# Kernel tuning notes

Hardware: AMD Instinct MI355X
Metric: run time of the kernel (lower is better)

Reference implementation:

```python
import jax, jax.numpy as jnp
import numpy as np

N_ATOMS = 100000
ATOM_FDIM = 133
HIDDEN = 512
MAX_NEI = 6
N_MOLS = 4096
N_PAIRS = 8192


def setup_inputs() -> dict:
    key = jax.random.key(0)
    ks = jax.random.split(key, 12)
    s = 0.05  # weight init scale
    return {
        'f_atoms': jax.random.normal(ks[0], (N_ATOMS, ATOM_FDIM), jnp.float32),
        'a_neighbors': jax.random.randint(ks[1], (N_ATOMS, MAX_NEI), 0, N_ATOMS, dtype=jnp.int32),
        'mol_ids': jnp.sort(jax.random.randint(ks[2], (N_ATOMS,), 0, N_MOLS, dtype=jnp.int32)),
        'batch_edges': jax.random.randint(ks[3], (2, N_PAIRS), 0, N_MOLS, dtype=jnp.int32),
        'W_i': jax.random.normal(ks[4], (ATOM_FDIM, HIDDEN), jnp.float32) * s,
        'W_h': jax.random.normal(ks[5], (HIDDEN, HIDDEN), jnp.float32) * s,
        'W_o': jax.random.normal(ks[6], (ATOM_FDIM + HIDDEN, HIDDEN), jnp.float32) * s,
        'b_o': jnp.zeros((HIDDEN,), jnp.float32),
        'W_ffn_i': jax.random.normal(ks[7], (4 * HIDDEN, 2048), jnp.float32) * s,
        'b_ffn_i': jnp.zeros((2048,), jnp.float32),
        'W_ffn_1': jax.random.normal(ks[8], (2048, 1024), jnp.float32) * s,
        'b_ffn_1': jnp.zeros((1024,), jnp.float32),
        'W_ffn_2': jax.random.normal(ks[9], (1024, 1), jnp.float32) * s,
        'b_ffn_2': jnp.zeros((1,), jnp.float32),
    }


def reference(f_atoms, a_neighbors, mol_ids, batch_edges,
              W_i, W_h, W_o, b_o,
              W_ffn_i, b_ffn_i, W_ffn_1, b_ffn_1, W_ffn_2, b_ffn_2):
    # input = W_i(f_atoms); message = relu(input)
    inp = f_atoms @ W_i                      # [N, H]
    message = jax.nn.relu(inp)
    # neighbor gather + sum aggregation
    message = jnp.take(message, a_neighbors, axis=0).sum(axis=1)  # [N, H]
    # single message-passing layer (n_message_layer = 1), dropout=0 -> identity
    message = jax.nn.relu(inp + message @ W_h)
    # second gather + sum, then readout projection
    a_message = jnp.take(message, a_neighbors, axis=0).sum(axis=1)  # [N, H]
    a_input = jnp.concatenate([f_atoms, a_message], axis=1)         # [N, F+H]
    atom_hiddens = jax.nn.relu(a_input @ W_o + b_o)                 # [N, H]
    # segment-mean readout per molecule (empty segments -> zero vector)
    sums = jax.ops.segment_sum(atom_hiddens, mol_ids, num_segments=N_MOLS)
    counts = jax.ops.segment_sum(jnp.ones((atom_hiddens.shape[0], 1), atom_hiddens.dtype),
                                 mol_ids, num_segments=N_MOLS)
    mol_vecs = sums / jnp.maximum(counts, 1.0)                      # [M, H]
    # pairwise drug-drug features
    e1 = mol_vecs[batch_edges[0]]
    e2 = mol_vecs[batch_edges[1]]
    feature = jnp.concatenate([e1 + e2, e1 * e2, e1, e2], axis=1)   # [P, 4H]
    h = feature @ W_ffn_i + b_ffn_i
    h = jax.nn.relu(h) @ W_ffn_1 + b_ffn_1
    h = jax.nn.relu(h) @ W_ffn_2 + b_ffn_2
    return jax.nn.sigmoid(h).reshape(-1)                            # [P]
```

## Files before the change

### kernel.cpp

```cpp
#include <hip/hip_runtime.h>
#include <math.h>

#define N_ATOMS   100000
#define ATOM_FDIM 133
#define HIDDEN    512
#define MAX_NEI   6
#define N_MOLS    4096
#define N_PAIRS   8192

typedef __attribute__((ext_vector_type(8))) short short8;
typedef __attribute__((ext_vector_type(4))) float f32x4;
typedef __attribute__((ext_vector_type(2))) float f32x2;
typedef __attribute__((ext_vector_type(8))) int int8v;

static __device__ __forceinline__ float bf2f(unsigned short h) {
    return __uint_as_float(((unsigned int)h) << 16);
}
static __device__ __forceinline__ unsigned short f2bf(float f) {
    unsigned int u = __float_as_uint(f);
    u += 0x7FFFu + ((u >> 16) & 1u);
    return (unsigned short)(u >> 16);
}
static __device__ __forceinline__ unsigned int pk2bf(float a, float b) {
    unsigned int ua = __float_as_uint(a); ua += 0x7FFFu + ((ua >> 16) & 1u);
    unsigned int ub = __float_as_uint(b); ub += 0x7FFFu + ((ub >> 16) & 1u);
    return (ua >> 16) | (ub & 0xFFFF0000u);
}
static __device__ __forceinline__ unsigned int pk4f8(float a, float b, float c, float d) {
    unsigned int r = 0;
    r = __builtin_amdgcn_cvt_pk_fp8_f32(a, b, r, false);
    r = __builtin_amdgcn_cvt_pk_fp8_f32(c, d, r, true);
    return r;
}
static __device__ __forceinline__ void gl_lds16(const void* g, void* l) {
    __builtin_amdgcn_global_load_lds(
        (__attribute__((address_space(1))) void*)g,
        (__attribute__((address_space(3))) void*)l, 16, 0, 0);
}

__global__ __launch_bounds__(256)
void convert_f8(const float* __restrict__ in, unsigned char* __restrict__ out)
{
    int v = blockIdx.x * 256 + threadIdx.x;
    int row = v >> 4, sl = v & 15;
    int k0 = sl * 16;
    bool rok = row < N_ATOMS;
    const float* r = in + (size_t)row * ATOM_FDIM;
    float f[16];
#pragma unroll
    for (int e = 0; e < 16; ++e) {
        int kk = k0 + e;
        f[e] = (rok && kk < ATOM_FDIM) ? r[kk] : 0.f;
    }
    uint4 u;
    u.x = pk4f8(f[0], f[1], f[2], f[3]);
    u.y = pk4f8(f[4], f[5], f[6], f[7]);
    u.z = pk4f8(f[8], f[9], f[10], f[11]);
    u.w = pk4f8(f[12], f[13], f[14], f[15]);
    *(uint4*)(out + (size_t)row * 256 + k0) = u;
}

template<bool HAS_A0, bool RELU, bool HAS_BIAS, bool HAS_ADD, bool SWZ>
__global__ __launch_bounds__(256)
void gemm_f8(const unsigned char* __restrict__ A0, int lda0, int K0p,
             const unsigned char* __restrict__ A2, int lda2, int Kp,
             const unsigned char* __restrict__ Bt,
             const float* __restrict__ bias,
             const unsigned char* __restrict__ addm,
             unsigned char* __restrict__ C, int M, int N)
{
    __shared__ unsigned char lds[128 * 256];
    unsigned char* As = lds;
    unsigned char* Bs = lds + 128 * 128;
    unsigned short* Ct = (unsigned short*)lds;

    const int tid  = threadIdx.x;
    const int lane = tid & 63;
    const int wid  = tid >> 6;
    int bx, by;
    if (SWZ) {
        int L = blockIdx.y * gridDim.x + blockIdx.x;
        int xcd = L & 7, s = L >> 3;
        bx = s % gridDim.x;
        by = xcd + 8 * (s / gridDim.x);
    } else { bx = blockIdx.x; by = blockIdx.y; }
    const int row0 = by * 128;
    const int col0 = bx * 128;
    const int wm   = wid & 1, wn = wid >> 1;
    const int quad = lane >> 4, l15 = lane & 15;
    const int srow = lane >> 3, schunk = lane & 7;
    const int ssw  = (schunk ^ srow) * 16;

    f32x4 acc[4][4];
#pragma unroll
    for (int i = 0; i < 4; ++i)
#pragma unroll
        for (int j = 0; j < 4; ++j)
#pragma unroll
            for (int r = 0; r < 4; ++r) acc[i][j][r] = 0.f;

    for (int k0 = 0; k0 < Kp; k0 += 128) {
        __syncthreads();
        const unsigned char* Ak;
        int akof, alda;
        if (HAS_A0 && k0 < K0p) { Ak = A0; akof = k0; alda = lda0; }
        else { Ak = A2; akof = HAS_A0 ? (k0 - K0p) : k0; alda = lda2; }
#pragma unroll
        for (int i = 0; i < 4; ++i) {
            int mbase = wid * 32 + i * 8;
            int r = row0 + mbase + srow;
            gl_lds16(Ak + (size_t)r * alda + akof + ssw, &As[mbase * 128]);
        }
#pragma unroll
        for (int i = 0; i < 4; ++i) {
            int nbase = wid * 32 + i * 8;
            int rn = col0 + nbase + srow;
            gl_lds16(Bt + (size_t)rn * Kp + k0 + ssw, &Bs[nbase * 128]);
        }
        __syncthreads();
        const int s0 = ((2 * quad) ^ (l15 & 7)) * 16;
        const int s1 = ((2 * quad + 1) ^ (l15 & 7)) * 16;
        int8v a[4], b[4];
#pragma unroll
        for (int mt = 0; mt < 4; ++mt) {
            int r = wm * 64 + mt * 16 + l15;
            uint4 lo = *(const uint4*)&As[r * 128 + s0];
            uint4 hi = *(const uint4*)&As[r * 128 + s1];
            a[mt][0] = lo.x; a[mt][1] = lo.y; a[mt][2] = lo.z; a[mt][3] = lo.w;
            a[mt][4] = hi.x; a[mt][5] = hi.y; a[mt][6] = hi.z; a[mt][7] = hi.w;
        }
#pragma unroll
        for (int nt = 0; nt < 4; ++nt) {
            int r = wn * 64 + nt * 16 + l15;
            uint4 lo = *(const uint4*)&Bs[r * 128 + s0];
            uint4 hi = *(const uint4*)&Bs[r * 128 + s1];
            b[nt][0] = lo.x; b[nt][1] = lo.y; b[nt][2] = lo.z; b[nt][3] = lo.w;
            b[nt][4] = hi.x; b[nt][5] = hi.y; b[nt][6] = hi.z; b[nt][7] = hi.w;
        }
#pragma unroll
        for (int mt = 0; mt < 4; ++mt)
#pragma unroll
            for (int nt = 0; nt < 4; ++nt)
                acc[mt][nt] = __builtin_amdgcn_mfma_scale_f32_16x16x128_f8f6f4(
                    a[mt], b[nt], acc[mt][nt], 0, 0, 0, 127, 0, 127);
    }

    __syncthreads();
#pragma unroll
    for (int mt = 0; mt < 4; ++mt)
#pragma unroll
        for (int nt = 0; nt < 4; ++nt) {
            int cbase = wn * 64 + nt * 16 + l15;
            int rbase = wm * 64 + mt * 16 + quad * 4;
#pragma unroll
            for (int r = 0; r < 4; ++r)
                Ct[(rbase + r) * 128 + cbase] = f2bf(acc[mt][nt][r]);
        }
    __syncthreads();
#pragma unroll
    for (int i = 0; i < 8; ++i) {
        int c = tid + i * 256;
        int rr = c >> 4, cc = (c & 15) * 8;
        int m = row0 + rr, n = col0 + cc;
        short8 v = *(const short8*)&Ct[rr * 128 + cc];
        float f[8];
#pragma unroll
        for (int q = 0; q < 8; ++q) f[q] = bf2f((unsigned short)v[q]);
        if (HAS_BIAS) {
            float4 b0 = *(const float4*)(bias + n);
            float4 b1 = *(const float4*)(bias + n + 4);
            f[0] += b0.x; f[1] += b0.y; f[2] += b0.z; f[3] += b0.w;
            f[4] += b1.x; f[5] += b1.y; f[6] += b1.z; f[7] += b1.w;
        }
        if (m < M) {
            if (HAS_ADD) {
                uint2 ad = *(const uint2*)(addm + (size_t)m * N + n);
                f32x2 p;
                p = __builtin_amdgcn_cvt_pk_f32_fp8(ad.x, false); f[0] += p.x; f[1] += p.y;
                p = __builtin_amdgcn_cvt_pk_f32_fp8(ad.x, true);  f[2] += p.x; f[3] += p.y;
                p = __builtin_amdgcn_cvt_pk_f32_fp8(ad.y, false); f[4] += p.x; f[5] += p.y;
                p = __builtin_amdgcn_cvt_pk_f32_fp8(ad.y, true);  f[6] += p.x; f[7] += p.y;
            }
            if (RELU)
#pragma unroll
                for (int q = 0; q < 8; ++q) f[q] = fmaxf(f[q], 0.f);
            uint2 o;
            o.x = pk4f8(f[0], f[1], f[2], f[3]);
            o.y = pk4f8(f[4], f[5], f[6], f[7]);
            *(uint2*)(C + (size_t)m * N + n) = o;
        }
    }
}

template<int NT, bool RELU, bool HAS_BIAS>
__global__ __launch_bounds__(512, 2)
void gemm_bt2(const unsigned short* __restrict__ A, int lda, int Kp,
              const unsigned short* __restrict__ Bt,
              const float* __restrict__ bias,
              unsigned short* __restrict__ C, int M, int N)
{
    constexpr int BN = NT * 64;
    constexpr int SMEM = 2 * 256 * 64 * 2 + 2 * BN * 64 * 2;
    __shared__ unsigned char smem[SMEM];
    unsigned short* As_ = (unsigned short*)smem;
    unsigned short* Bs_ = (unsigned short*)(smem + 2 * 256 * 64 * 2);
    unsigned short* Ct  = (unsigned short*)smem;

    const int tid  = threadIdx.x;
    const int lane = tid & 63;
    const int wid  = tid >> 6;
    const int wr   = wid >> 2;
    const int wc   = wid & 3;
    const int quad = lane >> 4, l15 = lane & 15;
    const int srow = lane >> 3, schunk = lane & 7;
    const int ssw  = (schunk ^ srow) * 8;

    const int row0 = blockIdx.y * 256;
    const int col0 = blockIdx.x * BN;

    f32x4 acc[8][NT];
#pragma unroll
    for (int i = 0; i < 8; ++i)
#pragma unroll
        for (int j = 0; j < NT; ++j)
#pragma unroll
            for (int r = 0; r < 4; ++r) acc[i][j][r] = 0.f;

#define STAGE_TILE(t, d)                                                     \
    {                                                                        \
        const int k0s = (t) * 64;                                            \
        _Pragma("unroll")                                                    \
        for (int i = 0; i < 4; ++i) {                                        \
            int mbase = wid * 32 + i * 8;                                    \
            int r = row0 + mbase + srow;                                     \
            gl_lds16(A + (size_t)r * lda + k0s + ssw,                        \
                     As_ + (d) * (256 * 64) + mbase * 64);                   \
        }                                                                    \
        _Pragma("unroll")                                                    \
        for (int i = 0; i < NT; ++i) {                                       \
            int nbase = wid * (NT * 8) + i * 8;                              \
            int rn = col0 + nbase + srow;                                    \
            gl_lds16(Bt + (size_t)rn * Kp + k0s + ssw,                       \
                     Bs_ + (d) * (BN * 64) + nbase * 64);                    \
        }                                                                    \
    }

    const int slot0 = ((quad) ^ (l15 & 7)) * 8;
    const int slot1 = ((4 + quad) ^ (l15 & 7)) * 8;

    const int ntiles = Kp >> 6;
    STAGE_TILE(0, 0);
    __syncthreads();

    for (int t = 0; t < ntiles; ++t) {
        const int d = t & 1;
        if (t + 1 < ntiles) STAGE_TILE(t + 1, d ^ 1);

        const int abase = d * (256 * 64);
        const int bbase = d * (BN * 64);
        short8 bf[NT][2];
#pragma unroll
        for (int nt2 = 0; nt2 < NT; ++nt2) {
            int cn = wc * (NT * 16) + nt2 * 16 + l15;
            bf[nt2][0] = *(const short8*)&Bs_[bbase + cn * 64 + slot0];
            bf[nt2][1] = *(const short8*)&Bs_[bbase + cn * 64 + slot1];
        }
#pragma unroll
        for (int q = 0; q < 4; ++q) {
            short8 af[2][2];
#pragma unroll
            for (int j = 0; j < 2; ++j) {
                int ar = wr * 128 + (q * 2 + j) * 16 + l15;
                af[j][0] = *(const short8*)&As_[abase + ar * 64 + slot0];
                af[j][1] = *(const short8*)&As_[abase + ar * 64 + slot1];
            }
            __builtin_amdgcn_s_setprio(1);
#pragma unroll
            for (int j = 0; j < 2; ++j)
#pragma unroll
                for (int nt2 = 0; nt2 < NT; ++nt2) {
                    acc[q * 2 + j][nt2] = __builtin_amdgcn_mfma_f32_16x16x32_bf16(
                        af[j][0], bf[nt2][0], acc[q * 2 + j][nt2], 0, 0, 0);
                    acc[q * 2 + j][nt2] = __builtin_amdgcn_mfma_f32_16x16x32_bf16(
                        af[j][1], bf[nt2][1], acc[q * 2 + j][nt2], 0, 0, 0);
                }
            __builtin_amdgcn_s_setprio(0);
        }
        __syncthreads();
    }
#undef STAGE_TILE

#pragma unroll
    for (int mt = 0; mt < 8; ++mt)
#pragma unroll
        for (int nt2 = 0; nt2 < NT; ++nt2) {
            int cbase = wc * (NT * 16) + nt2 * 16 + l15;
            int rbase = wr * 128 + mt * 16 + quad * 4;
#pragma unroll
            for (int r = 0; r < 4; ++r)
                Ct[(rbase + r) * BN + cbase] = f2bf(acc[mt][nt2][r]);
        }
    __syncthreads();
    constexpr int NSTORE = 256 * BN / (512 * 8);
#pragma unroll
    for (int i = 0; i < NSTORE; ++i) {
        int idx = (i * 512 + tid) * 8;
        int rr = idx / BN, cc = idx % BN;
        int m = row0 + rr, n = col0 + cc;
        short8 v = *(const short8*)&Ct[rr * BN + cc];
        float f[8];
#pragma unroll
        for (int q = 0; q < 8; ++q) f[q] = bf2f((unsigned short)v[q]);
        if (HAS_BIAS) {
            float4 b0 = *(const float4*)(bias + n);
            float4 b1 = *(const float4*)(bias + n + 4);
            f[0] += b0.x; f[1] += b0.y; f[2] += b0.z; f[3] += b0.w;
            f[4] += b1.x; f[5] += b1.y; f[6] += b1.z; f[7] += b1.w;
        }
        if (RELU)
#pragma unroll
            for (int q = 0; q < 8; ++q) f[q] = fmaxf(f[q], 0.f);
        uint4 o;
        o.x = pk2bf(f[0], f[1]); o.y = pk2bf(f[2], f[3]);
        o.z = pk2bf(f[4], f[5]); o.w = pk2bf(f[6], f[7]);
        *(uint4*)(C + (size_t)m * N + n) = o;
    }
    (void)M;
}

__global__ __launch_bounds__(256)
void transpose_bf16(const float* __restrict__ in, int K, int N,
                    unsigned short* __restrict__ out, int ldOut, int Kz, int koff)
{
    __shared__ float t[32][33];
    const int n0 = blockIdx.x * 32, k0 = blockIdx.y * 32;
    const int tx = threadIdx.x & 31, ty = threadIdx.x >> 5;
#pragma unroll
    for (int i = 0; i < 32; i += 8) {
        int k = k0 + ty + i, n = n0 + tx;
        t[ty + i][tx] = (k < K && n < N) ? in[(size_t)k * N + n] : 0.f;
    }
    __syncthreads();
#pragma unroll
    for (int i = 0; i < 32; i += 8) {
        int n = n0 + ty + i, k = k0 + tx;
        if (n < N && k < Kz)
            out[(size_t)n * ldOut + koff + k] = f2bf(t[tx][ty + i]);
    }
}

__global__ __launch_bounds__(256)
void transpose_f8(const float* __restrict__ in, int K, int N,
                  unsigned char* __restrict__ out, int ldOut, int Kz, int koff)
{
    __shared__ float t[32][33];
    const int n0 = blockIdx.x * 32, k0 = blockIdx.y * 32;
    const int tx = threadIdx.x & 31, ty = threadIdx.x >> 5;
#pragma unroll
    for (int i = 0; i < 32; i += 8) {
        int k = k0 + ty + i, n = n0 + tx;
        t[ty + i][tx] = (k < K && n < N) ? in[(size_t)k * N + n] : 0.f;
    }
    __syncthreads();
#pragma unroll
    for (int i = 0; i < 32; i += 8) {
        int n = n0 + ty + i, k = k0 + tx;
        if (n < N && k < Kz) {
            float v = t[tx][ty + i];
            out[(size_t)n * ldOut + koff + k] =
                (unsigned char)(__builtin_amdgcn_cvt_pk_fp8_f32(v, v, 0, false) & 0xFF);
        }
    }
}

__global__ __launch_bounds__(256)
void transpose_add_bf16(const float* __restrict__ inA, const float* __restrict__ inB,
                        int K, int N, unsigned short* __restrict__ out,
                        int ldOut, int koff)
{
    __shared__ float t[32][33];
    const int n0 = blockIdx.x * 32, k0 = blockIdx.y * 32;
    const int tx = threadIdx.x & 31, ty = threadIdx.x >> 5;
#pragma unroll
    for (int i = 0; i < 32; i += 8) {
        int k = k0 + ty + i, n = n0 + tx;
        float v = 0.f;
        if (k < K && n < N) {
            v = inA[(size_t)k * N + n];
            if (inB) v += inB[(size_t)k * N + n];
        }
        t[ty + i][tx] = v;
    }
    __syncthreads();
#pragma unroll
    for (int i = 0; i < 32; i += 8) {
        int n = n0 + ty + i, k = k0 + tx;
        if (n < N && k < K)
            out[(size_t)n * ldOut + koff + k] = f2bf(t[tx][ty + i]);
    }
}

template<bool RELU>
__global__ __launch_bounds__(256)
void gather_f8(const unsigned char* __restrict__ src,
               const int* __restrict__ nei, unsigned char* __restrict__ dst)
{
    const int atom = blockIdx.x * 8 + (threadIdx.x >> 5);
    const int l32  = threadIdx.x & 31;
    const int off  = l32 * 16;
    const int* np_ = nei + (size_t)atom * MAX_NEI;
    float s[16];
#pragma unroll
    for (int e = 0; e < 16; ++e) s[e] = 0.f;
#pragma unroll
    for (int j = 0; j < MAX_NEI; ++j) {
        uint4 u = *(const uint4*)(src + (size_t)np_[j] * HIDDEN + off);
        unsigned int w[4] = {u.x, u.y, u.z, u.w};
#pragma unroll
        for (int q = 0; q < 4; ++q) {
            f32x2 lo = __builtin_amdgcn_cvt_pk_f32_fp8(w[q], false);
            f32x2 hi = __builtin_amdgcn_cvt_pk_f32_fp8(w[q], true);
            float v0 = lo.x, v1 = lo.y, v2 = hi.x, v3 = hi.y;
            if (RELU) {
                v0 = fmaxf(v0, 0.f); v1 = fmaxf(v1, 0.f);
                v2 = fmaxf(v2, 0.f); v3 = fmaxf(v3, 0.f);
            }
            s[4 * q] += v0; s[4 * q + 1] += v1; s[4 * q + 2] += v2; s[4 * q + 3] += v3;
        }
    }
    uint4 o;
    o.x = pk4f8(s[0], s[1], s[2], s[3]);
    o.y = pk4f8(s[4], s[5], s[6], s[7]);
    o.z = pk4f8(s[8], s[9], s[10], s[11]);
    o.w = pk4f8(s[12], s[13], s[14], s[15]);
    *(uint4*)(dst + (size_t)atom * HIDDEN + off) = o;
}

__global__ __launch_bounds__(256)
void segmean_f8(const unsigned char* __restrict__ H,
                const int* __restrict__ mol_ids, float* __restrict__ molv)
{
    const int m = blockIdx.x;
    const int d = threadIdx.x * 2;
    int lo = 0, hi = N_ATOMS;
    while (lo < hi) { int mid = (lo + hi) >> 1; if (mol_ids[mid] < m) lo = mid + 1; else hi = mid; }
    const int start = lo;
    hi = N_ATOMS;
    while (lo < hi) { int mid = (lo + hi) >> 1; if (mol_ids[mid] < m + 1) lo = mid + 1; else hi = mid; }
    const int end = lo;
    float s0 = 0.f, s1 = 0.f;
    for (int a = start; a < end; ++a) {
        unsigned int raw = *(const unsigned short*)(H + (size_t)a * HIDDEN + d);
        f32x2 f = __builtin_amdgcn_cvt_pk_f32_fp8(raw, false);
        s0 += f.x; s1 += f.y;
    }
    int cnt = end - start;
    float inv = 1.0f / (float)(cnt > 0 ? cnt : 1);
    float2 o; o.x = s0 * inv; o.y = s1 * inv;
    *(float2*)(molv + (size_t)m * HIDDEN + d) = o;
}

__global__ __launch_bounds__(128)
void feature_kernel(const float* __restrict__ molv, const int* __restrict__ edges,
                    unsigned short* __restrict__ feat)
{
    const int p  = blockIdx.x;
    const int d4 = threadIdx.x * 4;
    const int i  = edges[p];
    const int j  = edges[N_PAIRS + p];
    float4 a = *(const float4*)(molv + (size_t)i * HIDDEN + d4);
    float4 b = *(const float4*)(molv + (size_t)j * HIDDEN + d4);
    unsigned short* o = feat + (size_t)p * 1536;
    uint2 w;
    w.x = pk2bf(a.x, a.y); w.y = pk2bf(a.z, a.w);
    *(uint2*)(o + d4) = w;
    w.x = pk2bf(b.x, b.y); w.y = pk2bf(b.z, b.w);
    *(uint2*)(o + HIDDEN + d4) = w;
    w.x = pk2bf(a.x * b.x, a.y * b.y); w.y = pk2bf(a.z * b.z, a.w * b.w);
    *(uint2*)(o + 2 * HIDDEN + d4) = w;
}

__global__ __launch_bounds__(256)
void final_kernel(const unsigned short* __restrict__ H, const float* __restrict__ w,
                  const float* __restrict__ b, float* __restrict__ out)
{
    const int p   = blockIdx.x;
    const int tid = threadIdx.x;
    const unsigned short* row = H + (size_t)p * 1024;
    float s = 0.f;
    for (int i = tid; i < 1024; i += 256) s += bf2f(row[i]) * w[i];
#pragma unroll
    for (int off = 32; off > 0; off >>= 1) s += __shfl_down(s, off, 64);
    __shared__ float red[4];
    if ((tid & 63) == 0) red[tid >> 6] = s;
    __syncthreads();
    if (tid == 0) {
        float t = red[0] + red[1] + red[2] + red[3] + b[0];
        out[p] = 1.0f / (1.0f + expf(-t));
    }
}

extern "C" void kernel_launch(void* const* d_in, const int* in_sizes, int n_in,
                              void* d_out, int out_size, void* d_ws, size_t ws_size,
                              hipStream_t stream)
{
    const float* f_atoms = (const float*)d_in[0];
    const int*   a_nei   = (const int*)d_in[1];
    const int*   mol_ids = (const int*)d_in[2];
    const int*   edges   = (const int*)d_in[3];
    const float* W_i     = (const float*)d_in[4];
    const float* W_h     = (const float*)d_in[5];
    const float* W_o     = (const float*)d_in[6];
    const float* b_o     = (const float*)d_in[7];
    const float* W_ffn_i = (const float*)d_in[8];
    const float* b_ffn_i = (const float*)d_in[9];
    const float* W_ffn_1 = (const float*)d_in[10];
    const float* b_ffn_1 = (const float*)d_in[11];
    const float* W_ffn_2 = (const float*)d_in[12];
    const float* b_ffn_2 = (const float*)d_in[13];
    float* out = (float*)d_out;

    char* ws = (char*)d_ws;
    unsigned char*  I     = (unsigned char*)ws;
    unsigned char*  Y     = (unsigned char*)(ws + 51200000);
    unsigned char*  Wt_i  = (unsigned char*)(ws + 102400000);
    unsigned char*  Wch   = (unsigned char*)(ws + 102531072);
    unsigned char*  Wco   = (unsigned char*)(ws + 102793216);
    float*          Mv    = (float*)(ws + 103186432);
    unsigned short* Wt_f0 = (unsigned short*)(ws + 111575040);
    unsigned short* Wt_f1 = (unsigned short*)(ws + 117866496);
    unsigned short* F     = (unsigned short*)(ws + 122060800);
    unsigned short* H1    = (unsigned short*)(ws + 147226624);
    unsigned short* H2    = (unsigned short*)(ws + 180781056);
    unsigned char*  Xf8   = (unsigned char*)(ws + 122060800);

    const float* W0 = W_ffn_i;
    const float* W1 = W_ffn_i + (size_t)512 * 2048;
    const float* W2 = W_ffn_i + (size_t)1024 * 2048;
    const float* W3 = W_ffn_i + (size_t)1536 * 2048;

    transpose_f8<<<dim3(16, 8),  256, 0, stream>>>(W_i, 133, 512, Wt_i, 256, 256, 0);
    transpose_f8<<<dim3(16, 16), 256, 0, stream>>>(W_h, 512, 512, Wch, 512, 512, 0);
    transpose_f8<<<dim3(16, 8),  256, 0, stream>>>(W_o, 133, 512, Wco, 768, 256, 0);
    transpose_f8<<<dim3(16, 16), 256, 0, stream>>>(W_o + (size_t)133 * 512,
                                                   512, 512, Wco, 768, 512, 256);
    transpose_add_bf16<<<dim3(64, 16), 256, 0, stream>>>(W0, W2, 512, 2048, Wt_f0, 1536, 0);
    transpose_add_bf16<<<dim3(64, 16), 256, 0, stream>>>(W0, W3, 512, 2048, Wt_f0, 1536, 512);
    transpose_add_bf16<<<dim3(64, 16), 256, 0, stream>>>(W1, nullptr, 512, 2048, Wt_f0, 1536, 1024);
    transpose_bf16<<<dim3(32, 64), 256, 0, stream>>>(W_ffn_1, 2048, 1024, Wt_f1, 2048, 2048, 0);

    convert_f8<<<100352 * 16 / 256, 256, 0, stream>>>(f_atoms, Xf8);

    gemm_f8<true, false, false, false, true><<<dim3(4, 784), 256, 0, stream>>>(
        Xf8, 256, 256, nullptr, 0, 256, Wt_i, nullptr, nullptr, I, N_ATOMS, HIDDEN);
    gather_f8<true><<<N_ATOMS / 8, 256, 0, stream>>>(I, a_nei, Y);
    gemm_f8<false, true, false, true, true><<<dim3(4, 784), 256, 0, stream>>>(
        nullptr, 0, 0, Y, 512, 512, Wch, nullptr, I, I, N_ATOMS, HIDDEN);
    gather_f8<false><<<N_ATOMS / 8, 256, 0, stream>>>(I, a_nei, Y);
    gemm_f8<true, true, true, false, true><<<dim3(4, 784), 256, 0, stream>>>(
        Xf8, 256, 256, Y, 512, 768, Wco, b_o, nullptr, I, N_ATOMS, HIDDEN);
    segmean_f8<<<N_MOLS, 256, 0, stream>>>(I, mol_ids, Mv);
    feature_kernel<<<N_PAIRS, 128, 0, stream>>>(Mv, edges, F);
    gemm_bt2<4, true, true><<<dim3(8, 32), 512, 0, stream>>>(
        F, 1536, 1536, Wt_f0, b_ffn_i, H1, N_PAIRS, 2048);
    gemm_bt2<2, true, true><<<dim3(8, 32), 512, 0, stream>>>(
        H1, 2048, 2048, Wt_f1, b_ffn_1, H2, N_PAIRS, 1024);
    final_kernel<<<N_PAIRS, 256, 0, stream>>>(H2, W_ffn_2, b_ffn_2, out);
    (void)in_sizes; (void)n_in; (void)out_size; (void)ws_size;
}
```

Before: 540.3 us.

## Double-buffer FP8 GEMM LDS tiles and remap bf16 GEMM blocks across XCDs

The FP8 GEMM now double-buffers its A/B LDS tiles (64KB), prefetching the next K tile while MFMAs run on the current one, with one barrier per iteration instead of two. It raises wave priority around the MFMA block and pads the bf16 output staging tile stride to 136 to reduce LDS bank conflicts. The bf16 GEMM remaps linear block IDs so consecutive tiles land on the same XCD for L2 locality. Doubling LDS use may lower occupancy, and the XCD remap assumes the grid size is divisible by 8.

```diff
diff --git a/kernel.cpp b/kernel.cpp
--- a/kernel.cpp
+++ b/kernel.cpp
@@ -69,9 +69,9 @@
              const unsigned char* __restrict__ addm,
              unsigned char* __restrict__ C, int M, int N)
 {
-    __shared__ unsigned char lds[128 * 256];
+    __shared__ unsigned char lds[65536];
     unsigned char* As = lds;
-    unsigned char* Bs = lds + 128 * 128;
+    unsigned char* Bs = lds + 32768;
     unsigned short* Ct = (unsigned short*)lds;
 
     const int tid  = threadIdx.x;
@@ -99,53 +99,70 @@
 #pragma unroll
             for (int r = 0; r < 4; ++r) acc[i][j][r] = 0.f;
 
-    for (int k0 = 0; k0 < Kp; k0 += 128) {
-        __syncthreads();
-        const unsigned char* Ak;
-        int akof, alda;
-        if (HAS_A0 && k0 < K0p) { Ak = A0; akof = k0; alda = lda0; }
-        else { Ak = A2; akof = HAS_A0 ? (k0 - K0p) : k0; alda = lda2; }
-#pragma unroll
-        for (int i = 0; i < 4; ++i) {
-            int mbase = wid * 32 + i * 8;
-            int r = row0 + mbase + srow;
-            gl_lds16(Ak + (size_t)r * alda + akof + ssw, &As[mbase * 128]);
-        }
-#pragma unroll
-        for (int i = 0; i < 4; ++i) {
-            int nbase = wid * 32 + i * 8;
-            int rn = col0 + nbase + srow;
-            gl_lds16(Bt + (size_t)rn * Kp + k0 + ssw, &Bs[nbase * 128]);
-        }
-        __syncthreads();
-        const int s0 = ((2 * quad) ^ (l15 & 7)) * 16;
-        const int s1 = ((2 * quad + 1) ^ (l15 & 7)) * 16;
+#define STAGE_F8(t, d)                                                        \
+    {                                                                         \
+        const int k0s = (t) * 128;                                            \
+        const unsigned char* Ak;                                              \
+        int akof, alda;                                                       \
+        if (HAS_A0 && k0s < K0p) { Ak = A0; akof = k0s; alda = lda0; }        \
+        else { Ak = A2; akof = HAS_A0 ? (k0s - K0p) : k0s; alda = lda2; }     \
+        _Pragma("unroll")                                                     \
+        for (int i = 0; i < 4; ++i) {                                         \
+            int mbase = wid * 32 + i * 8;                                     \
+            int r = row0 + mbase + srow;                                      \
+            gl_lds16(Ak + (size_t)r * alda + akof + ssw,                      \
+                     As + (d) * 16384 + mbase * 128);                         \
+        }                                                                     \
+        _Pragma("unroll")                                                     \
+        for (int i = 0; i < 4; ++i) {                                         \
+            int nbase = wid * 32 + i * 8;                                     \
+            int rn = col0 + nbase + srow;                                     \
+            gl_lds16(Bt + (size_t)rn * Kp + k0s + ssw,                        \
+                     Bs + (d) * 16384 + nbase * 128);                         \
+        }                                                                     \
+    }
+
+    const int ntiles = Kp >> 7;
+    STAGE_F8(0, 0);
+    __syncthreads();
+
+    const int s0 = ((2 * quad) ^ (l15 & 7)) * 16;
+    const int s1 = ((2 * quad + 1) ^ (l15 & 7)) * 16;
+
+    for (int t = 0; t < ntiles; ++t) {
+        const int d = t & 1;
+        if (t + 1 < ntiles) STAGE_F8(t + 1, d ^ 1);
+        const int ab = d * 16384;
+
         int8v a[4], b[4];
 #pragma unroll
         for (int mt = 0; mt < 4; ++mt) {
             int r = wm * 64 + mt * 16 + l15;
-            uint4 lo = *(const uint4*)&As[r * 128 + s0];
-            uint4 hi = *(const uint4*)&As[r * 128 + s1];
+            uint4 lo = *(const uint4*)&As[ab + r * 128 + s0];
+            uint4 hi = *(const uint4*)&As[ab + r * 128 + s1];
             a[mt][0] = lo.x; a[mt][1] = lo.y; a[mt][2] = lo.z; a[mt][3] = lo.w;
             a[mt][4] = hi.x; a[mt][5] = hi.y; a[mt][6] = hi.z; a[mt][7] = hi.w;
         }
 #pragma unroll
         for (int nt = 0; nt < 4; ++nt) {
             int r = wn * 64 + nt * 16 + l15;
-            uint4 lo = *(const uint4*)&Bs[r * 128 + s0];
-            uint4 hi = *(const uint4*)&Bs[r * 128 + s1];
+            uint4 lo = *(const uint4*)&Bs[ab + r * 128 + s0];
+            uint4 hi = *(const uint4*)&Bs[ab + r * 128 + s1];
             b[nt][0] = lo.x; b[nt][1] = lo.y; b[nt][2] = lo.z; b[nt][3] = lo.w;
             b[nt][4] = hi.x; b[nt][5] = hi.y; b[nt][6] = hi.z; b[nt][7] = hi.w;
         }
+        __builtin_amdgcn_s_setprio(1);
 #pragma unroll
         for (int mt = 0; mt < 4; ++mt)
 #pragma unroll
             for (int nt = 0; nt < 4; ++nt)
                 acc[mt][nt] = __builtin_amdgcn_mfma_scale_f32_16x16x128_f8f6f4(
                     a[mt], b[nt], acc[mt][nt], 0, 0, 0, 127, 0, 127);
-    }
-
-    __syncthreads();
+        __builtin_amdgcn_s_setprio(0);
+        __syncthreads();
+    }
+#undef STAGE_F8
+
 #pragma unroll
     for (int mt = 0; mt < 4; ++mt)
 #pragma unroll
@@ -154,7 +171,7 @@
             int rbase = wm * 64 + mt * 16 + quad * 4;
 #pragma unroll
             for (int r = 0; r < 4; ++r)
-                Ct[(rbase + r) * 128 + cbase] = f2bf(acc[mt][nt][r]);
+                Ct[(rbase + r) * 136 + cbase] = f2bf(acc[mt][nt][r]);
         }
     __syncthreads();
 #pragma unroll
@@ -162,7 +179,7 @@
         int c = tid + i * 256;
         int rr = c >> 4, cc = (c & 15) * 8;
         int m = row0 + rr, n = col0 + cc;
-        short8 v = *(const short8*)&Ct[rr * 128 + cc];
+        short8 v = *(const short8*)&Ct[rr * 136 + cc];
         float f[8];
 #pragma unroll
         for (int q = 0; q < 8; ++q) f[q] = bf2f((unsigned short)v[q]);
@@ -215,8 +232,11 @@
     const int srow = lane >> 3, schunk = lane & 7;
     const int ssw  = (schunk ^ srow) * 8;
 
-    const int row0 = blockIdx.y * 256;
-    const int col0 = blockIdx.x * BN;
+    const int L = blockIdx.y * gridDim.x + blockIdx.x;
+    const int chunk = (gridDim.x * gridDim.y) >> 3;
+    const int Ls = (L & 7) * chunk + (L >> 3);
+    const int row0 = (Ls / gridDim.x) * 256;
+    const int col0 = (Ls % gridDim.x) * BN;
 
     f32x4 acc[8][NT];
 #pragma unroll
```

Measured after the change: 572.1 us. 1.06x slower.
